# Performance work log

Hardware: AMD Instinct MI355X
Metric: run time of the kernel (lower is better)

Reference implementation:

```python
import jax, jax.numpy as jnp
import numpy as np

B, S, D, H = 4, 2048, 1024, 16
DK = D // H


def setup_inputs() -> dict:
    key = jax.random.key(0)
    ks = jax.random.split(key, 5)
    scale = 1.0 / np.sqrt(D)
    return {
        "x": jax.random.normal(ks[0], (B, S, D), dtype=jnp.float32),
        "mask": jnp.ones((1, 1, S, S), dtype=bool),
        "Wq": jax.random.normal(ks[1], (D, D), dtype=jnp.float32) * scale,
        "Wk": jax.random.normal(ks[2], (D, D), dtype=jnp.float32) * scale,
        "Wv": jax.random.normal(ks[3], (D, D), dtype=jnp.float32) * scale,
        "Wo": jax.random.normal(ks[4], (D, D), dtype=jnp.float32) * scale,
    }


def reference(x, mask, Wq, Wk, Wv, Wo):
    # nn.Linear(d_model, d_model, bias=False): y = x @ W.T
    q = jnp.einsum('bsd,ed->bse', x, Wq).reshape(B, S, H, DK).transpose(0, 2, 1, 3)
    k = jnp.einsum('bsd,ed->bse', x, Wk).reshape(B, S, H, DK).transpose(0, 2, 1, 3)
    v = jnp.einsum('bsd,ed->bse', x, Wv).reshape(B, S, H, DK).transpose(0, 2, 1, 3)
    # scaled dot-product attention: [B,H,S,S]
    scores = jnp.einsum('bhqd,bhkd->bhqk', q, k) / jnp.sqrt(jnp.float32(DK))
    scores = jnp.where(mask, scores, jnp.float32(-1e9))
    attn = jax.nn.softmax(scores, axis=-1)
    out = jnp.einsum('bhqk,bhkd->bhqd', attn, v)  # [B,H,S,DK]
    out = out.transpose(0, 2, 1, 3).reshape(B, S, D)
    return jnp.einsum('bsd,ed->bse', out, Wo)
```

## Files before the change

kernel.cpp:

```cpp
#include <hip/hip_runtime.h>

typedef __bf16 bf16x8 __attribute__((ext_vector_type(8)));
typedef float f32x4 __attribute__((ext_vector_type(4)));
typedef float f32x16 __attribute__((ext_vector_type(16)));
typedef unsigned short u16;
typedef unsigned short u16x8 __attribute__((ext_vector_type(8)));
typedef unsigned short u16x4 __attribute__((ext_vector_type(4)));
typedef unsigned int u32;
typedef unsigned int u32x4 __attribute__((ext_vector_type(4)));

#define MFMA16(a, b, c) __builtin_amdgcn_mfma_f32_16x16x32_bf16(a, b, c, 0, 0, 0)
#define MFMA32(a, b, c) __builtin_amdgcn_mfma_f32_32x32x16_bf16(a, b, c, 0, 0, 0)

#if defined(__has_builtin)
#if __has_builtin(__builtin_amdgcn_exp2f)
#define EXP2(x) __builtin_amdgcn_exp2f(x)
#endif
#endif
#ifndef EXP2
#define EXP2(x) exp2f(x)
#endif

constexpr int NB = 4, NH = 16, SEQ = 2048, DM = 1024, DKH = 64;
constexpr int MTOT = NB * SEQ;
constexpr size_t QKV_ELEMS = (size_t)MTOT * DM;
constexpr size_t W_ELEMS = (size_t)DM * DM;
constexpr float QSCALE = 0.125f * 1.44269504088896340736f;

__device__ __forceinline__ int swz(int row, int col, int rowlen) {
  return (row * rowlen + col) ^ ((row & 7) << 3);
}

__device__ __forceinline__ void gload16(const u16* g, u16* l) {
  __builtin_amdgcn_global_load_lds(
      (const __attribute__((address_space(1))) void*)g,
      (__attribute__((address_space(3))) void*)l, 16, 0, 0);
}

__device__ __forceinline__ u32 cvtpk(float lo, float hi) {
  u32 r;
  asm("v_cvt_pk_bf16_f32 %0, %1, %2" : "=v"(r) : "v"(lo), "v"(hi));
  return r;
}
__device__ __forceinline__ void plswap(u32& a, u32& b) {
  asm volatile("v_permlane32_swap_b32 %0, %1" : "+v"(a), "+v"(b));
}

__global__ __launch_bounds__(256) void convert_bf16(
    const float* __restrict__ X, const float* __restrict__ Wq,
    const float* __restrict__ Wk, const float* __restrict__ Wv,
    const float* __restrict__ Wo, u16* __restrict__ Xb,
    u16* __restrict__ Wqb, u16* __restrict__ Wkb, u16* __restrict__ Wvb,
    u16* __restrict__ Wob) {
  const int bid = blockIdx.x;
  const float* src;
  u16* dst;
  size_t base;
  if (bid < 4096) {
    src = X; dst = Xb; base = (size_t)bid * 2048;
  } else {
    const int t = (bid - 4096) >> 9, r = (bid - 4096) & 511;
    src = (t == 0) ? Wq : (t == 1) ? Wk : (t == 2) ? Wv : Wo;
    dst = (t == 0) ? Wqb : (t == 1) ? Wkb : (t == 2) ? Wvb : Wob;
    base = (size_t)r * 2048;
  }
  const size_t e = base + (size_t)threadIdx.x * 8;
  const float4 a = *reinterpret_cast<const float4*>(src + e);
  const float4 b = *reinterpret_cast<const float4*>(src + e + 4);
  bf16x8 v;
  v[0] = (__bf16)a.x; v[1] = (__bf16)a.y; v[2] = (__bf16)a.z; v[3] = (__bf16)a.w;
  v[4] = (__bf16)b.x; v[5] = (__bf16)b.y; v[6] = (__bf16)b.z; v[7] = (__bf16)b.w;
  *reinterpret_cast<bf16x8*>(dst + e) = v;
}

__global__ __launch_bounds__(256) void gemm_qkv(
    const u16* __restrict__ A, const u16* __restrict__ Wqb,
    const u16* __restrict__ Wkb, const u16* __restrict__ Wvb,
    u16* __restrict__ Qb, u16* __restrict__ Kb, u16* __restrict__ Vtb) {
  constexpr int BM = 128, BK = 64, NT = DM / BK;
  __shared__ __align__(16) u16 As[2][BM * BK];
  __shared__ __align__(16) u16 Bs[2][BM * BK];

  const int mode = blockIdx.y >> 3;
  const u16* B = (mode == 0) ? Wqb : (mode == 1) ? Wkb : Wvb;
  u16* Yz = (mode == 0) ? Qb : (mode == 1) ? Kb : Vtb;

  const int tid = threadIdx.x;
  const int lane = tid & 63, w = tid >> 6;
  const int ln = lane & 15, lg = lane >> 4;
  const int wr = (w >> 1) * 64, wc = (w & 1) * 64;
  const int m0 = blockIdx.x * BM, n0 = (blockIdx.y & 7) * BM;

  const int srow = tid >> 3;
  const int sgg = (tid & 7) ^ (srow & 7);
  const size_t aoff = (size_t)(m0 + srow) * DM + sgg * 8;
  const size_t boff = (size_t)(n0 + srow) * DM + sgg * 8;
  const int lbase = w * 512;

  f32x4 acc[4][4];
#pragma unroll
  for (int i = 0; i < 4; ++i)
#pragma unroll
    for (int j = 0; j < 4; ++j) acc[i][j] = (f32x4){0.f, 0.f, 0.f, 0.f};

  auto stage = [&](int bsel, int k0) {
#pragma unroll
    for (int c = 0; c < 4; ++c) {
      gload16(A + aoff + (size_t)c * 32 * DM + k0, &As[bsel][c * 2048 + lbase]);
      gload16(B + boff + (size_t)c * 32 * DM + k0, &Bs[bsel][c * 2048 + lbase]);
    }
  };

  stage(0, 0);
  __syncthreads();

  int buf = 0;
  for (int t = 0; t < NT; ++t) {
    if (t + 1 < NT) stage(buf ^ 1, (t + 1) * BK);
    if (mode == 2) {
#pragma unroll
      for (int kc = 0; kc < 2; ++kc) {
        bf16x8 af[4], bfr[4];
#pragma unroll
        for (int i = 0; i < 4; ++i)
          af[i] = *reinterpret_cast<const bf16x8*>(
              &As[buf][swz(wr + i * 16 + ln, kc * 32 + lg * 8, BK)]);
#pragma unroll
        for (int j = 0; j < 4; ++j)
          bfr[j] = *reinterpret_cast<const bf16x8*>(
              &Bs[buf][swz(wc + j * 16 + ln, kc * 32 + lg * 8, BK)]);
#pragma unroll
        for (int i = 0; i < 4; ++i)
#pragma unroll
          for (int j = 0; j < 4; ++j) acc[i][j] = MFMA16(af[i], bfr[j], acc[i][j]);
      }
    } else {
#pragma unroll
      for (int kc = 0; kc < 2; ++kc) {
        bf16x8 af[4], bfr[4];
#pragma unroll
        for (int i = 0; i < 4; ++i)
          af[i] = *reinterpret_cast<const bf16x8*>(
              &As[buf][swz(wr + i * 16 + ln, kc * 32 + lg * 8, BK)]);
#pragma unroll
        for (int j = 0; j < 4; ++j)
          bfr[j] = *reinterpret_cast<const bf16x8*>(
              &Bs[buf][swz(wc + j * 16 + ln, kc * 32 + lg * 8, BK)]);
#pragma unroll
        for (int i = 0; i < 4; ++i)
#pragma unroll
          for (int j = 0; j < 4; ++j) acc[i][j] = MFMA16(bfr[j], af[i], acc[i][j]);
      }
    }
    __syncthreads();
    buf ^= 1;
  }

  if (mode == 2) {
#pragma unroll
    for (int i = 0; i < 4; ++i) {
      const int mB = m0 + wr + i * 16 + lg * 4;
      const int bb = mB >> 11, s0 = mB & (SEQ - 1);
#pragma unroll
      for (int j = 0; j < 4; ++j) {
        const int n = n0 + wc + j * 16 + ln;
        const int h = n >> 6, dk = n & 63;
        u16x4 ov;
#pragma unroll
        for (int r = 0; r < 4; ++r)
          ov[r] = __builtin_bit_cast(u16, (__bf16)acc[i][j][r]);
        *reinterpret_cast<u16x4*>(
            &Yz[(((size_t)(bb * NH + h)) * DKH + dk) * SEQ + s0]) = ov;
      }
    }
  } else {
    const float sc = (mode == 0) ? QSCALE : 1.0f;
#pragma unroll
    for (int i = 0; i < 4; ++i) {
      const int m = m0 + wr + i * 16 + ln;
      const int bb = m >> 11, s = m & (SEQ - 1);
#pragma unroll
      for (int j = 0; j < 4; ++j) {
        const int nb = n0 + wc + j * 16 + lg * 4;
        const int h = nb >> 6, dk0 = nb & 63;
        u16x4 ov;
#pragma unroll
        for (int r = 0; r < 4; ++r)
          ov[r] = __builtin_bit_cast(u16, (__bf16)(acc[i][j][r] * sc));
        *reinterpret_cast<u16x4*>(
            &Yz[(((size_t)(bb * NH + h)) * SEQ + s) * DKH + dk0]) = ov;
      }
    }
  }
}

__global__ __launch_bounds__(256) void gemm_out(
    const u16* __restrict__ A, const u16* __restrict__ B,
    float* __restrict__ Out) {
  constexpr int BM = 128, BK = 64, NT = DM / BK;
  __shared__ __align__(16) u16 As[2][BM * BK];
  __shared__ __align__(16) u16 Bs[2][BM * BK];

  const int tid = threadIdx.x;
  const int lane = tid & 63, w = tid >> 6;
  const int ln = lane & 15, lg = lane >> 4;
  const int wr = (w >> 1) * 64, wc = (w & 1) * 64;
  const int m0 = blockIdx.x * BM, n0 = blockIdx.y * BM;

  const int srow = tid >> 3;
  const int sgg = (tid & 7) ^ (srow & 7);
  const size_t aoff = (size_t)(m0 + srow) * DM + sgg * 8;
  const size_t boff = (size_t)(n0 + srow) * DM + sgg * 8;
  const int lbase = w * 512;

  f32x4 acc[4][4];
#pragma unroll
  for (int i = 0; i < 4; ++i)
#pragma unroll
    for (int j = 0; j < 4; ++j) acc[i][j] = (f32x4){0.f, 0.f, 0.f, 0.f};

  auto stage = [&](int bsel, int k0) {
#pragma unroll
    for (int c = 0; c < 4; ++c) {
      gload16(A + aoff + (size_t)c * 32 * DM + k0, &As[bsel][c * 2048 + lbase]);
      gload16(B + boff + (size_t)c * 32 * DM + k0, &Bs[bsel][c * 2048 + lbase]);
    }
  };

  stage(0, 0);
  __syncthreads();

  int buf = 0;
  for (int t = 0; t < NT; ++t) {
    if (t + 1 < NT) stage(buf ^ 1, (t + 1) * BK);
#pragma unroll
    for (int kc = 0; kc < 2; ++kc) {
      bf16x8 af[4], bfr[4];
#pragma unroll
      for (int i = 0; i < 4; ++i)
        af[i] = *reinterpret_cast<const bf16x8*>(
            &As[buf][swz(wr + i * 16 + ln, kc * 32 + lg * 8, BK)]);
#pragma unroll
      for (int j = 0; j < 4; ++j)
        bfr[j] = *reinterpret_cast<const bf16x8*>(
            &Bs[buf][swz(wc + j * 16 + ln, kc * 32 + lg * 8, BK)]);
#pragma unroll
      for (int i = 0; i < 4; ++i)
#pragma unroll
        for (int j = 0; j < 4; ++j) acc[i][j] = MFMA16(bfr[j], af[i], acc[i][j]);
    }
    __syncthreads();
    buf ^= 1;
  }

#pragma unroll
  for (int i = 0; i < 4; ++i) {
    const int m = m0 + wr + i * 16 + ln;
#pragma unroll
    for (int j = 0; j < 4; ++j) {
      const int nb = n0 + wc + j * 16 + lg * 4;
      float4 v = {acc[i][j][0], acc[i][j][1], acc[i][j][2], acc[i][j][3]};
      *reinterpret_cast<float4*>(&Out[(size_t)m * DM + nb]) = v;
    }
  }
}

__global__ __launch_bounds__(512, 4) void attn_fwd(
    const u16* __restrict__ Qg, const u16* __restrict__ Kg,
    const u16* __restrict__ Vg, u16* __restrict__ Og) {
  constexpr int KVB = 64, NT = SEQ / KVB;
  const int bid = blockIdx.x;
  const int xcd = bid & 7, grp = bid >> 3;
  const int bh = xcd * 8 + (grp >> 3), qt = grp & 7;
  const int b = bh >> 4, h = bh & 15;
  const int tid = threadIdx.x, lane = tid & 63, wv = tid >> 6;
  const int l31 = lane & 31, hi = lane >> 5;
  const size_t hoff = (size_t)bh * SEQ * DKH;
  const u16* __restrict__ Qh = Qg + hoff;
  const u16* __restrict__ Kh = Kg + hoff;
  const u16* __restrict__ Vth = Vg + hoff;

  __shared__ __align__(16) u16 Ks[4][8 * 512];
  __shared__ __align__(16) u16 Vs[4][8 * 512];

  const int qbase = qt * 256 + wv * 32;

  bf16x8 qf[4];
#pragma unroll
  for (int c = 0; c < 4; ++c)
    qf[c] = *reinterpret_cast<const bf16x8*>(
        Qh + (size_t)(qbase + l31) * DKH + c * 16 + hi * 8);

  f32x16 ot0, ot1;
  f32x4 lv;
#pragma unroll
  for (int i = 0; i < 16; ++i) { ot0[i] = 0.f; ot1[i] = 0.f; }
#pragma unroll
  for (int i = 0; i < 4; ++i) lv[i] = 0.f;

  const u16* sK = Kh + (size_t)((wv >> 2) * 32 + l31) * DKH + (wv & 3) * 16 + hi * 8;
  const u16* sV = Vth + (size_t)((wv >> 2) * 32 + l31) * SEQ + (wv & 3) * 16 + hi * 8;

  auto stage = [&](int bsel, int kv0) {
    gload16(sK + (size_t)kv0 * DKH, &Ks[bsel][wv * 512]);
    gload16(sV + kv0, &Vs[bsel][wv * 512]);
  };

  stage(0, 0);
  asm volatile("" ::: "memory");
  stage(1, KVB);
  asm volatile("" ::: "memory");
  stage(2, 2 * KVB);

  int cur = 0;
  for (int t = 0; t < NT; ++t) {
    if (t < NT - 2) asm volatile("s_waitcnt vmcnt(4)" ::: "memory");
    else if (t == NT - 2) asm volatile("s_waitcnt vmcnt(2)" ::: "memory");
    else asm volatile("s_waitcnt vmcnt(0)" ::: "memory");
    __builtin_amdgcn_s_barrier();
    if (t + 3 < NT) stage((cur + 3) & 3, (t + 3) * KVB);

    const u16* ksb = Ks[cur];
    const u16* vsb = Vs[cur];

    f32x16 sf[2];
#pragma unroll
    for (int i = 0; i < 16; ++i) { sf[0][i] = 0.f; sf[1][i] = 0.f; }

    __builtin_amdgcn_s_setprio(1);
#pragma unroll
    for (int ks = 0; ks < 2; ++ks)
#pragma unroll
      for (int c = 0; c < 4; ++c) {
        bf16x8 ka = *reinterpret_cast<const bf16x8*>(
            &ksb[(ks * 4 + c) * 512 + lane * 8]);
        sf[ks] = MFMA32(ka, qf[c], sf[ks]);
      }
    __builtin_amdgcn_s_setprio(0);

#pragma unroll
    for (int ks = 0; ks < 2; ++ks)
#pragma unroll
      for (int i = 0; i < 16; ++i) sf[ks][i] = EXP2(sf[ks][i]);
#pragma unroll
    for (int i = 0; i < 4; ++i)
      lv[i] += ((sf[0][i] + sf[0][i + 4]) + (sf[0][i + 8] + sf[0][i + 12])) +
               ((sf[1][i] + sf[1][i + 4]) + (sf[1][i + 8] + sf[1][i + 12]));

#pragma unroll
    for (int ks = 0; ks < 2; ++ks) {
#pragma unroll
      for (int hk = 0; hk < 2; ++hk) {
        u32 wA0 = cvtpk(sf[ks][8 * hk + 0], sf[ks][8 * hk + 1]);
        u32 wA1 = cvtpk(sf[ks][8 * hk + 2], sf[ks][8 * hk + 3]);
        u32 wB0 = cvtpk(sf[ks][8 * hk + 4], sf[ks][8 * hk + 5]);
        u32 wB1 = cvtpk(sf[ks][8 * hk + 6], sf[ks][8 * hk + 7]);
        plswap(wA0, wB0);
        plswap(wA1, wB1);
        u32x4 pw;
        pw[0] = wA0; pw[1] = wA1; pw[2] = wB0; pw[3] = wB1;
        const bf16x8 pb = __builtin_bit_cast(bf16x8, pw);
        const int kc = ks * 2 + hk;
        __builtin_amdgcn_s_setprio(1);
        bf16x8 va0 = *reinterpret_cast<const bf16x8*>(
            &vsb[kc * 512 + lane * 8]);
        bf16x8 va1 = *reinterpret_cast<const bf16x8*>(
            &vsb[(4 + kc) * 512 + lane * 8]);
        ot0 = MFMA32(va0, pb, ot0);
        ot1 = MFMA32(va1, pb, ot1);
        __builtin_amdgcn_s_setprio(0);
      }
    }

    cur = (cur + 1) & 3;
  }

  float l = (lv[0] + lv[1]) + (lv[2] + lv[3]);
  l += __shfl_xor(l, 32);
  const float inv = 1.f / l;
  const int q = qbase + l31;
#pragma unroll
  for (int ds = 0; ds < 2; ++ds)
#pragma unroll
    for (int blk = 0; blk < 4; ++blk) {
      u16x4 ov;
#pragma unroll
      for (int r = 0; r < 4; ++r) {
        const float o = (ds == 0 ? ot0[blk * 4 + r] : ot1[blk * 4 + r]) * inv;
        ov[r] = __builtin_bit_cast(u16, (__bf16)o);
      }
      const int d0 = ds * 32 + blk * 8 + hi * 4;
      *reinterpret_cast<u16x4*>(
          &Og[((size_t)(b * SEQ + q)) * DM + h * DKH + d0]) = ov;
    }
}

extern "C" void kernel_launch(void* const* d_in, const int* in_sizes, int n_in,
                              void* d_out, int out_size, void* d_ws, size_t ws_size,
                              hipStream_t stream) {
  const float* x  = (const float*)d_in[0];
  const float* Wq = (const float*)d_in[2];
  const float* Wk = (const float*)d_in[3];
  const float* Wv = (const float*)d_in[4];
  const float* Wo = (const float*)d_in[5];
  float* out = (float*)d_out;

  u16* Xb  = (u16*)d_ws;
  u16* Wqb = Xb + QKV_ELEMS;
  u16* Wkb = Wqb + W_ELEMS;
  u16* Wvb = Wkb + W_ELEMS;
  u16* Wob = Wvb + W_ELEMS;
  u16* Kb  = Wob + W_ELEMS;
  u16* Vtb = Kb + QKV_ELEMS;
  u16* Qb  = (u16*)d_out;
  u16* Obuf = Xb;

  convert_bf16<<<6144, 256, 0, stream>>>(x, Wq, Wk, Wv, Wo,
                                         Xb, Wqb, Wkb, Wvb, Wob);
  gemm_qkv<<<dim3(MTOT / 128, 24), 256, 0, stream>>>(Xb, Wqb, Wkb, Wvb,
                                                     Qb, Kb, Vtb);
  attn_fwd<<<dim3(NB * NH * 8), 512, 0, stream>>>(Qb, Kb, Vtb, Obuf);
  gemm_out<<<dim3(MTOT / 128, DM / 128), 256, 0, stream>>>(Obuf, Wob, out);
}
```

Measured before the change: 186.2 us.

## Restructure attention KV pipeline to stage tile pairs with one barrier per pair

Replaces the 4-deep per-tile prefetch ring (one wait and barrier per KV tile, three tiles in flight) with a pair-based schedule. Two tiles are staged at a time, the kernel waits for all loads, issues the next pair, then computes both tiles. This halves the number of barriers and waitcnt points but reduces prefetch depth. Each pair's loads must fully land before compute starts, which risks exposing more global-load latency.

```diff
diff --git a/kernel.cpp b/kernel.cpp
--- a/kernel.cpp
+++ b/kernel.cpp
@@ -268,7 +268,7 @@
 __global__ __launch_bounds__(512, 4) void attn_fwd(
     const u16* __restrict__ Qg, const u16* __restrict__ Kg,
     const u16* __restrict__ Vg, u16* __restrict__ Og) {
-  constexpr int KVB = 64, NT = SEQ / KVB;
+  constexpr int KVB = 64, NT = SEQ / KVB, NP = NT / 2;
   const int bid = blockIdx.x;
   const int xcd = bid & 7, grp = bid >> 3;
   const int bh = xcd * 8 + (grp >> 3), qt = grp & 7;
@@ -305,23 +305,15 @@
     gload16(sK + (size_t)kv0 * DKH, &Ks[bsel][wv * 512]);
     gload16(sV + kv0, &Vs[bsel][wv * 512]);
   };
-
-  stage(0, 0);
-  asm volatile("" ::: "memory");
-  stage(1, KVB);
-  asm volatile("" ::: "memory");
-  stage(2, 2 * KVB);
-
-  int cur = 0;
-  for (int t = 0; t < NT; ++t) {
-    if (t < NT - 2) asm volatile("s_waitcnt vmcnt(4)" ::: "memory");
-    else if (t == NT - 2) asm volatile("s_waitcnt vmcnt(2)" ::: "memory");
-    else asm volatile("s_waitcnt vmcnt(0)" ::: "memory");
-    __builtin_amdgcn_s_barrier();
-    if (t + 3 < NT) stage((cur + 3) & 3, (t + 3) * KVB);
-
-    const u16* ksb = Ks[cur];
-    const u16* vsb = Vs[cur];
+  auto stagePair = [&](int p) {
+    const int t0 = 2 * p;
+    stage(t0 & 3, t0 * KVB);
+    stage((t0 + 1) & 3, (t0 + 1) * KVB);
+  };
+
+  auto tile = [&](int t) {
+    const u16* ksb = Ks[t & 3];
+    const u16* vsb = Vs[t & 3];
 
     f32x16 sf[2];
 #pragma unroll
@@ -371,8 +363,15 @@
         __builtin_amdgcn_s_setprio(0);
       }
     }
-
-    cur = (cur + 1) & 3;
+  };
+
+  stagePair(0);
+  for (int p = 0; p < NP; ++p) {
+    asm volatile("s_waitcnt vmcnt(0)" ::: "memory");
+    __builtin_amdgcn_s_barrier();
+    if (p + 1 < NP) stagePair(p + 1);
+    tile(2 * p);
+    tile(2 * p + 1);
   }
 
   float l = (lv[0] + lv[1]) + (lv[2] + lv[3]);
```

After: 188.8 us. Within noise of the previous version (+1.4%).

## Replace GEMMs with 256x256 8-wave ping-pong pipelined templated kernel

Applied to the files above, without the earlier changes.

Replaces the 128x128 QKV and output-projection GEMMs with a templated 256x256-tile, 512-thread kernel that uses 128 KB of dynamic LDS. The K loop is split into quarter-tile phases that interleave LDS fragment reads, global-to-LDS staging and MFMA bursts, separated by raw barriers and explicit vmcnt waits, with s_setprio around the MFMA bursts. The aim is more data reuse per tile and better overlap of memory traffic with MFMA work. In exchange, the fused QKV launch becomes three separate launches of 128 blocks each, which fills fewer CUs per launch and leaves one block per CU.

```diff
diff --git a/kernel.cpp b/kernel.cpp
--- a/kernel.cpp
+++ b/kernel.cpp
@@ -44,6 +44,9 @@
 }
 __device__ __forceinline__ void plswap(u32& a, u32& b) {
   asm volatile("v_permlane32_swap_b32 %0, %1" : "+v"(a), "+v"(b));
+}
+__device__ __forceinline__ void barrier_raw() {
+  asm volatile("s_barrier" ::: "memory");
 }
 
 __global__ __launch_bounds__(256) void convert_bf16(
@@ -73,97 +76,137 @@
   *reinterpret_cast<bf16x8*>(dst + e) = v;
 }
 
-__global__ __launch_bounds__(256) void gemm_qkv(
-    const u16* __restrict__ A, const u16* __restrict__ Wqb,
-    const u16* __restrict__ Wkb, const u16* __restrict__ Wvb,
-    u16* __restrict__ Qb, u16* __restrict__ Kb, u16* __restrict__ Vtb) {
-  constexpr int BM = 128, BK = 64, NT = DM / BK;
-  __shared__ __align__(16) u16 As[2][BM * BK];
-  __shared__ __align__(16) u16 Bs[2][BM * BK];
-
-  const int mode = blockIdx.y >> 3;
-  const u16* B = (mode == 0) ? Wqb : (mode == 1) ? Wkb : Wvb;
-  u16* Yz = (mode == 0) ? Qb : (mode == 1) ? Kb : Vtb;
-
+template <int MODE>
+__global__ __launch_bounds__(512, 1) void gemm8(
+    const u16* __restrict__ A, const u16* __restrict__ B,
+    u16* __restrict__ Yz, float* __restrict__ Out) {
+  constexpr int BM = 256, BK = 64, NIT = DM / BK / 2;
+  extern __shared__ __align__(16) u16 smem[];
   const int tid = threadIdx.x;
-  const int lane = tid & 63, w = tid >> 6;
+  const int lane = tid & 63, wid = tid >> 6;
+  const int wm = wid >> 2, wn = wid & 3;
   const int ln = lane & 15, lg = lane >> 4;
-  const int wr = (w >> 1) * 64, wc = (w & 1) * 64;
-  const int m0 = blockIdx.x * BM, n0 = (blockIdx.y & 7) * BM;
+  const int m0 = blockIdx.x * BM;
+  const int n0 = (MODE == 3 ? blockIdx.y : (blockIdx.y & 3)) * 256;
 
   const int srow = tid >> 3;
-  const int sgg = (tid & 7) ^ (srow & 7);
-  const size_t aoff = (size_t)(m0 + srow) * DM + sgg * 8;
-  const size_t boff = (size_t)(n0 + srow) * DM + sgg * 8;
-  const int lbase = w * 512;
-
-  f32x4 acc[4][4];
-#pragma unroll
-  for (int i = 0; i < 4; ++i)
+  const int sg = (tid & 7) ^ (srow & 7);
+  const int ldst = srow * 64 + (tid & 7) * 8;
+
+  f32x4 acc[8][4];
+#pragma unroll
+  for (int i = 0; i < 8; ++i)
 #pragma unroll
     for (int j = 0; j < 4; ++j) acc[i][j] = (f32x4){0.f, 0.f, 0.f, 0.f};
 
-  auto stage = [&](int bsel, int k0) {
-#pragma unroll
-    for (int c = 0; c < 4; ++c) {
-      gload16(A + aoff + (size_t)c * 32 * DM + k0, &As[bsel][c * 2048 + lbase]);
-      gload16(B + boff + (size_t)c * 32 * DM + k0, &Bs[bsel][c * 2048 + lbase]);
+  auto stageA = [&](int buf, int h, int k0) {
+    const u16* src = A + (size_t)(m0 + h * 128 + srow) * DM + k0 + sg * 8;
+    u16* dst = smem + (size_t)(buf * 2 + h) * 8192 + ldst;
+    gload16(src, dst);
+    gload16(src + (size_t)64 * DM, dst + 64 * 64);
+  };
+  auto stageB = [&](int buf, int h, int k0) {
+    const u16* src = B + (size_t)(n0 + h * 128 + srow) * DM + k0 + sg * 8;
+    u16* dst = smem + (size_t)(4 + buf * 2 + h) * 8192 + ldst;
+    gload16(src, dst);
+    gload16(src + (size_t)64 * DM, dst + 64 * 64);
+  };
+
+  bf16x8 am0[4][2], am1[4][2], b0f[2][2], b1f[2][2];
+  auto dsA = [&](bf16x8(&dst)[4][2], int buf, int mh) {
+    const u16* ah = smem + (size_t)(buf * 2 + wm) * 8192;
+#pragma unroll
+    for (int i = 0; i < 4; ++i)
+#pragma unroll
+      for (int kc = 0; kc < 2; ++kc)
+        dst[i][kc] = *reinterpret_cast<const bf16x8*>(
+            &ah[swz(mh * 64 + i * 16 + ln, kc * 32 + lg * 8, 64)]);
+  };
+  auto dsB = [&](bf16x8(&dst)[2][2], int buf, int nh) {
+    const u16* bh = smem + (size_t)(4 + buf * 2 + (wn >> 1)) * 8192;
+#pragma unroll
+    for (int j = 0; j < 2; ++j)
+#pragma unroll
+      for (int kc = 0; kc < 2; ++kc)
+        dst[j][kc] = *reinterpret_cast<const bf16x8*>(
+            &bh[swz((wn & 1) * 64 + (nh * 2 + j) * 16 + ln,
+                    kc * 32 + lg * 8, 64)]);
+  };
+  auto mmac = [&](bf16x8(&af)[4][2], bf16x8(&bfr)[2][2], int mh, int nh) {
+    __builtin_amdgcn_s_setprio(1);
+#pragma unroll
+    for (int i = 0; i < 4; ++i)
+#pragma unroll
+      for (int j = 0; j < 2; ++j)
+#pragma unroll
+        for (int kc = 0; kc < 2; ++kc) {
+          if constexpr (MODE == 2)
+            acc[mh * 4 + i][nh * 2 + j] =
+                MFMA16(af[i][kc], bfr[j][kc], acc[mh * 4 + i][nh * 2 + j]);
+          else
+            acc[mh * 4 + i][nh * 2 + j] =
+                MFMA16(bfr[j][kc], af[i][kc], acc[mh * 4 + i][nh * 2 + j]);
+        }
+    __builtin_amdgcn_s_setprio(0);
+  };
+
+#pragma unroll
+  for (int h = 0; h < 2; ++h) { stageA(0, h, 0); stageB(0, h, 0); }
+#pragma unroll
+  for (int h = 0; h < 2; ++h) { stageA(1, h, BK); stageB(1, h, BK); }
+  asm volatile("s_waitcnt vmcnt(0)" ::: "memory");
+  barrier_raw();
+
+  for (int I = 0; I < NIT; ++I) {
+    const int a = 2 * I;
+    const bool last = (I == NIT - 1);
+    dsA(am0, 0, 0); dsB(b0f, 0, 0);
+    if (I > 0) stageB(1, 0, (a + 1) * BK);
+    barrier_raw(); mmac(am0, b0f, 0, 0); barrier_raw();
+    dsA(am1, 0, 1);
+    if (I > 0) stageB(1, 1, (a + 1) * BK);
+    barrier_raw(); mmac(am1, b0f, 1, 0); barrier_raw();
+    dsB(b1f, 0, 1);
+    if (!last) stageA(0, 0, (a + 2) * BK);
+    barrier_raw(); mmac(am1, b1f, 1, 1); barrier_raw();
+    if (!last) stageA(0, 1, (a + 2) * BK);
+    if (last) asm volatile("s_waitcnt vmcnt(0)" ::: "memory");
+    else      asm volatile("s_waitcnt vmcnt(4)" ::: "memory");
+    barrier_raw(); mmac(am0, b1f, 0, 1); barrier_raw();
+    dsA(am0, 1, 0); dsB(b0f, 1, 0);
+    if (!last) stageB(0, 0, (a + 2) * BK);
+    barrier_raw(); mmac(am0, b0f, 0, 0); barrier_raw();
+    dsA(am1, 1, 1);
+    if (!last) stageB(0, 1, (a + 2) * BK);
+    barrier_raw(); mmac(am1, b0f, 1, 0); barrier_raw();
+    dsB(b1f, 1, 1);
+    if (!last) stageA(1, 0, (a + 3) * BK);
+    barrier_raw(); mmac(am1, b1f, 1, 1); barrier_raw();
+    if (!last) stageA(1, 1, (a + 3) * BK);
+    if (I >= NIT - 2) asm volatile("s_waitcnt vmcnt(0)" ::: "memory");
+    else              asm volatile("s_waitcnt vmcnt(4)" ::: "memory");
+    barrier_raw(); mmac(am0, b1f, 0, 1); barrier_raw();
+  }
+
+  if constexpr (MODE == 3) {
+#pragma unroll
+    for (int i = 0; i < 8; ++i) {
+      const int m = m0 + wm * 128 + i * 16 + ln;
+#pragma unroll
+      for (int j = 0; j < 4; ++j) {
+        const int nb = n0 + wn * 64 + j * 16 + lg * 4;
+        float4 v = {acc[i][j][0], acc[i][j][1], acc[i][j][2], acc[i][j][3]};
+        *reinterpret_cast<float4*>(&Out[(size_t)m * DM + nb]) = v;
+      }
     }
-  };
-
-  stage(0, 0);
-  __syncthreads();
-
-  int buf = 0;
-  for (int t = 0; t < NT; ++t) {
-    if (t + 1 < NT) stage(buf ^ 1, (t + 1) * BK);
-    if (mode == 2) {
-#pragma unroll
-      for (int kc = 0; kc < 2; ++kc) {
-        bf16x8 af[4], bfr[4];
-#pragma unroll
-        for (int i = 0; i < 4; ++i)
-          af[i] = *reinterpret_cast<const bf16x8*>(
-              &As[buf][swz(wr + i * 16 + ln, kc * 32 + lg * 8, BK)]);
-#pragma unroll
-        for (int j = 0; j < 4; ++j)
-          bfr[j] = *reinterpret_cast<const bf16x8*>(
-              &Bs[buf][swz(wc + j * 16 + ln, kc * 32 + lg * 8, BK)]);
-#pragma unroll
-        for (int i = 0; i < 4; ++i)
-#pragma unroll
-          for (int j = 0; j < 4; ++j) acc[i][j] = MFMA16(af[i], bfr[j], acc[i][j]);
-      }
-    } else {
-#pragma unroll
-      for (int kc = 0; kc < 2; ++kc) {
-        bf16x8 af[4], bfr[4];
-#pragma unroll
-        for (int i = 0; i < 4; ++i)
-          af[i] = *reinterpret_cast<const bf16x8*>(
-              &As[buf][swz(wr + i * 16 + ln, kc * 32 + lg * 8, BK)]);
-#pragma unroll
-        for (int j = 0; j < 4; ++j)
-          bfr[j] = *reinterpret_cast<const bf16x8*>(
-              &Bs[buf][swz(wc + j * 16 + ln, kc * 32 + lg * 8, BK)]);
-#pragma unroll
-        for (int i = 0; i < 4; ++i)
-#pragma unroll
-          for (int j = 0; j < 4; ++j) acc[i][j] = MFMA16(bfr[j], af[i], acc[i][j]);
-      }
-    }
-    __syncthreads();
-    buf ^= 1;
-  }
-
-  if (mode == 2) {
-#pragma unroll
-    for (int i = 0; i < 4; ++i) {
-      const int mB = m0 + wr + i * 16 + lg * 4;
+  } else if constexpr (MODE == 2) {
+#pragma unroll
+    for (int i = 0; i < 8; ++i) {
+      const int mB = m0 + wm * 128 + i * 16 + lg * 4;
       const int bb = mB >> 11, s0 = mB & (SEQ - 1);
 #pragma unroll
       for (int j = 0; j < 4; ++j) {
-        const int n = n0 + wc + j * 16 + ln;
+        const int n = n0 + wn * 64 + j * 16 + ln;
         const int h = n >> 6, dk = n & 63;
         u16x4 ov;
 #pragma unroll
@@ -174,14 +217,14 @@
       }
     }
   } else {
-    const float sc = (mode == 0) ? QSCALE : 1.0f;
-#pragma unroll
-    for (int i = 0; i < 4; ++i) {
-      const int m = m0 + wr + i * 16 + ln;
+    const float sc = (MODE == 0) ? QSCALE : 1.0f;
+#pragma unroll
+    for (int i = 0; i < 8; ++i) {
+      const int m = m0 + wm * 128 + i * 16 + ln;
       const int bb = m >> 11, s = m & (SEQ - 1);
 #pragma unroll
       for (int j = 0; j < 4; ++j) {
-        const int nb = n0 + wc + j * 16 + lg * 4;
+        const int nb = n0 + wn * 64 + j * 16 + lg * 4;
         const int h = nb >> 6, dk0 = nb & 63;
         u16x4 ov;
 #pragma unroll
@@ -190,77 +233,6 @@
         *reinterpret_cast<u16x4*>(
             &Yz[(((size_t)(bb * NH + h)) * SEQ + s) * DKH + dk0]) = ov;
       }
-    }
-  }
-}
-
-__global__ __launch_bounds__(256) void gemm_out(
-    const u16* __restrict__ A, const u16* __restrict__ B,
-    float* __restrict__ Out) {
-  constexpr int BM = 128, BK = 64, NT = DM / BK;
-  __shared__ __align__(16) u16 As[2][BM * BK];
-  __shared__ __align__(16) u16 Bs[2][BM * BK];
-
-  const int tid = threadIdx.x;
-  const int lane = tid & 63, w = tid >> 6;
-  const int ln = lane & 15, lg = lane >> 4;
-  const int wr = (w >> 1) * 64, wc = (w & 1) * 64;
-  const int m0 = blockIdx.x * BM, n0 = blockIdx.y * BM;
-
-  const int srow = tid >> 3;
-  const int sgg = (tid & 7) ^ (srow & 7);
-  const size_t aoff = (size_t)(m0 + srow) * DM + sgg * 8;
-  const size_t boff = (size_t)(n0 + srow) * DM + sgg * 8;
-  const int lbase = w * 512;
-
-  f32x4 acc[4][4];
-#pragma unroll
-  for (int i = 0; i < 4; ++i)
-#pragma unroll
-    for (int j = 0; j < 4; ++j) acc[i][j] = (f32x4){0.f, 0.f, 0.f, 0.f};
-
-  auto stage = [&](int bsel, int k0) {
-#pragma unroll
-    for (int c = 0; c < 4; ++c) {
-      gload16(A + aoff + (size_t)c * 32 * DM + k0, &As[bsel][c * 2048 + lbase]);
-      gload16(B + boff + (size_t)c * 32 * DM + k0, &Bs[bsel][c * 2048 + lbase]);
-    }
-  };
-
-  stage(0, 0);
-  __syncthreads();
-
-  int buf = 0;
-  for (int t = 0; t < NT; ++t) {
-    if (t + 1 < NT) stage(buf ^ 1, (t + 1) * BK);
-#pragma unroll
-    for (int kc = 0; kc < 2; ++kc) {
-      bf16x8 af[4], bfr[4];
-#pragma unroll
-      for (int i = 0; i < 4; ++i)
-        af[i] = *reinterpret_cast<const bf16x8*>(
-            &As[buf][swz(wr + i * 16 + ln, kc * 32 + lg * 8, BK)]);
-#pragma unroll
-      for (int j = 0; j < 4; ++j)
-        bfr[j] = *reinterpret_cast<const bf16x8*>(
-            &Bs[buf][swz(wc + j * 16 + ln, kc * 32 + lg * 8, BK)]);
-#pragma unroll
-      for (int i = 0; i < 4; ++i)
-#pragma unroll
-        for (int j = 0; j < 4; ++j) acc[i][j] = MFMA16(bfr[j], af[i], acc[i][j]);
-    }
-    __syncthreads();
-    buf ^= 1;
-  }
-
-#pragma unroll
-  for (int i = 0; i < 4; ++i) {
-    const int m = m0 + wr + i * 16 + ln;
-#pragma unroll
-    for (int j = 0; j < 4; ++j) {
-      const int nb = n0 + wc + j * 16 + lg * 4;
-      float4 v = {acc[i][j][0], acc[i][j][1], acc[i][j][2], acc[i][j][3]};
-      *reinterpret_cast<float4*>(&Out[(size_t)m * DM + nb]) = v;
     }
   }
 }
@@ -415,10 +387,25 @@
   u16* Qb  = (u16*)d_out;
   u16* Obuf = Xb;
 
+  constexpr int LDS8 = 8 * 8192 * (int)sizeof(u16);
+  static bool attr_done = false;
+  if (!attr_done) {
+    (void)hipFuncSetAttribute((const void*)gemm8<0>,
+        hipFuncAttributeMaxDynamicSharedMemorySize, LDS8);
+    (void)hipFuncSetAttribute((const void*)gemm8<1>,
+        hipFuncAttributeMaxDynamicSharedMemorySize, LDS8);
+    (void)hipFuncSetAttribute((const void*)gemm8<2>,
+        hipFuncAttributeMaxDynamicSharedMemorySize, LDS8);
+    (void)hipFuncSetAttribute((const void*)gemm8<3>,
+        hipFuncAttributeMaxDynamicSharedMemorySize, LDS8);
+    attr_done = true;
+  }
+
   convert_bf16<<<6144, 256, 0, stream>>>(x, Wq, Wk, Wv, Wo,
                                          Xb, Wqb, Wkb, Wvb, Wob);
-  gemm_qkv<<<dim3(MTOT / 128, 24), 256, 0, stream>>>(Xb, Wqb, Wkb, Wvb,
-                                                     Qb, Kb, Vtb);
+  gemm8<0><<<dim3(MTOT / 256, 4), 512, LDS8, stream>>>(Xb, Wqb, Qb, nullptr);
+  gemm8<1><<<dim3(MTOT / 256, 4), 512, LDS8, stream>>>(Xb, Wkb, Kb, nullptr);
+  gemm8<2><<<dim3(MTOT / 256, 4), 512, LDS8, stream>>>(Xb, Wvb, Vtb, nullptr);
   attn_fwd<<<dim3(NB * NH * 8), 512, 0, stream>>>(Qb, Kb, Vtb, Obuf);
-  gemm_out<<<dim3(MTOT / 128, DM / 128), 256, 0, stream>>>(Obuf, Wob, out);
-}
+  gemm8<3><<<dim3(MTOT / 256, 4), 512, LDS8, stream>>>(Obuf, Wob, nullptr, out);
+}
```

After: 265.8 us. 42.8% more time.
